# Optimization experiments

Hardware: AMD Instinct MI355X
Metric: run time of the kernel (lower is better)

The kernel has to match this reference:

```python
import jax, jax.numpy as jnp
import numpy as np

B, HH, WW = 4, 192, 192
DIM, HEADS, WIN, SHIFT, HID = 256, 8, 8, 4, 1024
EPS = 1e-5


def _rel_index(w):
    coords = np.stack(np.meshgrid(np.arange(w), np.arange(w), indexing='ij')).reshape(2, -1)
    rel = coords[:, :, None] - coords[:, None, :]            # [2, N, N]
    rel = rel.transpose(1, 2, 0).astype(np.int64)
    rel[:, :, 0] += w - 1
    rel[:, :, 1] += w - 1
    rel[:, :, 0] *= 2 * w - 1
    return rel.sum(-1)                                        # [N, N]


def _ln(x, g, b):
    m = x.mean(-1, keepdims=True)
    v = ((x - m) ** 2).mean(-1, keepdims=True)
    return (x - m) / jnp.sqrt(v + EPS) * g + b


def setup_inputs() -> dict:
    key = jax.random.key(0)
    ks = jax.random.split(key, 8)
    s = 0.02
    return {
        'x': jax.random.normal(ks[0], (B, HH * WW, DIM), jnp.float32),
        'norm1_g': jnp.ones((DIM,), jnp.float32),
        'norm1_b': jnp.zeros((DIM,), jnp.float32),
        'qkv_w': s * jax.random.normal(ks[1], (DIM, 3 * DIM), jnp.float32),
        'qkv_b': jnp.zeros((3 * DIM,), jnp.float32),
        'bias_table': s * jax.random.normal(ks[2], ((2 * WIN - 1) ** 2, HEADS), jnp.float32),
        'proj_w': s * jax.random.normal(ks[3], (DIM, DIM), jnp.float32),
        'proj_b': jnp.zeros((DIM,), jnp.float32),
        'norm2_g': jnp.ones((DIM,), jnp.float32),
        'norm2_b': jnp.zeros((DIM,), jnp.float32),
        'fc1_w': s * jax.random.normal(ks[4], (DIM, HID), jnp.float32),
        'fc1_b': jnp.zeros((HID,), jnp.float32),
        'fc2_w': s * jax.random.normal(ks[5], (HID, DIM), jnp.float32),
        'fc2_b': jnp.zeros((DIM,), jnp.float32),
        'H': HH,
        'W': WW,
    }


def reference(x, norm1_g, norm1_b, qkv_w, qkv_b, bias_table, proj_w, proj_b,
              norm2_g, norm2_b, fc1_w, fc1_b, fc2_w, fc2_b, H, W):
    Bn, L, C = x.shape
    hd = C // HEADS
    win = min(WIN, H, W)
    shift = SHIFT if win > SHIFT else 0
    shortcut = x

    h = _ln(x, norm1_g, norm1_b).reshape(Bn, H, W, C)
    pad_b = (win - H % win) % win
    pad_r = (win - W % win) % win
    h = jnp.pad(h, ((0, 0), (0, pad_b), (0, pad_r), (0, 0)))
    Hp, Wp = H + pad_b, W + pad_r
    if shift > 0:
        h = jnp.roll(h, (-shift, -shift), axis=(1, 2))

    nh, nw = Hp // win, Wp // win
    h = h.reshape(Bn, nh, win, nw, win, C).transpose(0, 1, 3, 2, 4, 5)
    h = h.reshape(Bn * nh * nw, win * win, C)
    N = win * win

    # windowed attention
    qkv = (h @ qkv_w + qkv_b).reshape(-1, N, 3, HEADS, hd)
    q, k, v = qkv[:, :, 0], qkv[:, :, 1], qkv[:, :, 2]      # [Bw, N, H, hd]
    scale = hd ** -0.5
    attn = jnp.einsum('bqhd,bkhd->bhqk', q * scale, k)
    rel_idx = jnp.asarray(_rel_index(win))                   # [N, N]
    bias = bias_table[rel_idx.reshape(-1)].reshape(N, N, HEADS).transpose(2, 0, 1)
    attn = jax.nn.softmax(attn + bias[None], axis=-1)
    o = jnp.einsum('bhqk,bkhd->bqhd', attn, v).reshape(-1, N, C)
    o = o @ proj_w + proj_b

    # window reverse
    o = o.reshape(Bn, nh, nw, win, win, C).transpose(0, 1, 3, 2, 4, 5).reshape(Bn, Hp, Wp, C)
    if shift > 0:
        o = jnp.roll(o, (shift, shift), axis=(1, 2))
    o = o[:, :H, :W, :].reshape(Bn, H * W, C)

    x = shortcut + o
    m = _ln(x, norm2_g, norm2_b)
    m = jax.nn.gelu(m @ fc1_w + fc1_b, approximate=False) @ fc2_w + fc2_b
    return x + m
```

## Files before the change

### kernel.cpp

```cpp
#include <hip/hip_runtime.h>


#define SHIFT_ 4

typedef __attribute__((ext_vector_type(8))) short short8;
typedef __attribute__((ext_vector_type(4))) float floatx4;

__device__ __forceinline__ unsigned short f2b(float f) {
  union { float f; unsigned int i; } c; c.f = f;
  unsigned int u = c.i;
  return (unsigned short)((u + 0x7FFFu + ((u >> 16) & 1u)) >> 16);
}

__device__ __forceinline__ float fast_gelu(float v) {
  const float u = v * v;
  const float z = v * (2.3022082f + 0.10294326f * u);
  const float e = __builtin_amdgcn_exp2f(z);
  const float r = __builtin_amdgcn_rcpf(1.f + e);
  return v - v * r;
}

__device__ __forceinline__ void load_lds16(const void* g, void* l) {
  __builtin_amdgcn_global_load_lds((__attribute__((address_space(1))) void*)g,
                                   (__attribute__((address_space(3))) void*)l, 16, 0, 0);
}

__device__ __forceinline__ size_t tok_of_row(int row) {
  int widx = row >> 6, t = row & 63;
  int b = widx / 576; int rem = widx - b * 576;
  int wy = rem / 24, wx = rem - wy * 24;
  int ti = t >> 3, tj = t & 7;
  int gr = wy * 8 + ti + SHIFT_; if (gr >= 192) gr -= 192;
  int gc = wx * 8 + tj + SHIFT_; if (gc >= 192) gc -= 192;
  return (size_t)b * 36864 + (size_t)(gr * 192 + gc);
}

template<int SHUFFLE>
__global__ __launch_bounds__(256) void ln_kernel(const float* __restrict__ src,
    const float* __restrict__ gw, const float* __restrict__ bw,
    unsigned short* __restrict__ dst) {
  const int lane = threadIdx.x & 63;
  const int m = blockIdx.x * 4 + (threadIdx.x >> 6);
  const size_t soff = SHUFFLE ? tok_of_row(m) * 256 : (size_t)m * 256;
  float4 xv = *(const float4*)(src + soff + lane * 4);
  float s  = xv.x + xv.y + xv.z + xv.w;
  float s2 = xv.x * xv.x + xv.y * xv.y + xv.z * xv.z + xv.w * xv.w;
  #pragma unroll
  for (int off = 32; off > 0; off >>= 1) { s += __shfl_xor(s, off); s2 += __shfl_xor(s2, off); }
  const float mean = s * 0.00390625f;
  const float var  = s2 * 0.00390625f - mean * mean;
  const float rstd = rsqrtf(var + 1e-5f);
  float4 gv = *(const float4*)(gw + lane * 4);
  float4 bv = *(const float4*)(bw + lane * 4);
  ushort4 o;
  o.x = f2b((xv.x - mean) * rstd * gv.x + bv.x);
  o.y = f2b((xv.y - mean) * rstd * gv.y + bv.y);
  o.z = f2b((xv.z - mean) * rstd * gv.z + bv.z);
  o.w = f2b((xv.w - mean) * rstd * gv.w + bv.w);
  *(ushort4*)(dst + (size_t)m * 256 + lane * 4) = o;
}

__global__ void wconv(const float* __restrict__ W, unsigned short* __restrict__ Wt,
                      int K, int N) {
  const int idx = blockIdx.x * 256 + threadIdx.x;
  const int n = idx / K, k = idx - n * K;
  Wt[idx] = f2b(W[(size_t)k * N + n]);
}

template<int MODE>
__global__ __launch_bounds__(256) void gemm_bt(
    const unsigned short* __restrict__ A, const unsigned short* __restrict__ Wt,
    const float* __restrict__ bias, const float* __restrict__ X,
    unsigned short* __restrict__ outb, float* __restrict__ outf,
    int Ntot, int K) {
  __shared__ unsigned short sm[16384];
  const int tid = threadIdx.x;
  const int wave = tid >> 6, lane = tid & 63;
  const int lr = lane & 15, lg = lane >> 4;
  const int wm = wave >> 1, wn = wave & 1;
  const int m0 = blockIdx.y * 128, n0 = blockIdx.x * 128;

  const unsigned short* rbase = (wave < 2) ? (A + (size_t)m0 * K)
                                           : (Wt + (size_t)n0 * K);
  unsigned short* ldsbase = &sm[wave * 4096];
  const int rc0 = (wave & 1) * 8;
  int off[8];
  #pragma unroll
  for (int t = 0; t < 8; ++t) {
    const int P = (rc0 + t) * 64 + lane;
    const int r = P >> 3, c = (P & 7) ^ (r & 7);
    off[t] = r * K + c * 8;
  }

  floatx4 acc[4][4];
  #pragma unroll
  for (int i = 0; i < 4; ++i)
    #pragma unroll
    for (int j = 0; j < 4; ++j) acc[i][j] = (floatx4)0.f;

  for (int k0 = 0; k0 < K; k0 += 64) {
    __syncthreads();
    #pragma unroll
    for (int t = 0; t < 8; ++t)
      load_lds16(rbase + (off[t] + k0), ldsbase + t * 512);
    __syncthreads();
    #pragma unroll
    for (int kk = 0; kk < 2; ++kk) {
      short8 af[4], bf[4];
      #pragma unroll
      for (int mi = 0; mi < 4; ++mi) {
        const int r = wm * 64 + mi * 16 + lr;
        af[mi] = *(const short8*)&sm[r * 64 + (((kk * 4 + lg) ^ (r & 7)) * 8)];
      }
      #pragma unroll
      for (int ni = 0; ni < 4; ++ni) {
        const int r = wn * 64 + ni * 16 + lr;
        bf[ni] = *(const short8*)&sm[8192 + r * 64 + (((kk * 4 + lg) ^ (r & 7)) * 8)];
      }
      #pragma unroll
      for (int mi = 0; mi < 4; ++mi)
        #pragma unroll
        for (int ni = 0; ni < 4; ++ni)
          acc[mi][ni] = __builtin_amdgcn_mfma_f32_16x16x32_bf16(af[mi], bf[ni], acc[mi][ni], 0, 0, 0);
    }
  }

  #pragma unroll
  for (int mi = 0; mi < 4; ++mi) {
    #pragma unroll
    for (int r = 0; r < 4; ++r) {
      const int row = m0 + wm * 64 + mi * 16 + lg * 4 + r;
      size_t obase;
      if (MODE == 1) obase = tok_of_row(row) * 256;
      else obase = (size_t)row * Ntot;
      #pragma unroll
      for (int ni = 0; ni < 4; ++ni) {
        const int col = n0 + wn * 64 + ni * 16 + lr;
        const float v = acc[mi][ni][r] + bias[col];
        if (MODE == 0) {
          outb[obase + col] = f2b(v);
        } else if (MODE == 1) {
          outf[obase + col] = X[obase + col] + v;
        } else if (MODE == 2) {
          outb[obase + col] = f2b(fast_gelu(v));
        } else {
          outf[obase + col] = X[obase + col] + v;
        }
      }
    }
  }
}

__global__ __launch_bounds__(64) void attn_kernel(const unsigned short* __restrict__ qkv,
    const float* __restrict__ btab, unsigned short* __restrict__ obuf) {
  __shared__ unsigned short vts[2048];
  __shared__ unsigned short ps[4096];
  __shared__ float bs[225];
  const int l = threadIdx.x;
  const int win = blockIdx.x >> 3, head = blockIdx.x & 7;
  const int lr = l & 15, lg = l >> 4;
  const unsigned short* base = qkv + (size_t)(win * 64) * 768 + head * 32;

  #pragma unroll
  for (int c = 0; c < 8; ++c) {
    ushort4 vv = *(const ushort4*)(base + (size_t)l * 768 + 512 + c * 4);
    #pragma unroll
    for (int j = 0; j < 4; ++j) {
      const int d = c * 4 + j;
      const unsigned short val = j == 0 ? vv.x : j == 1 ? vv.y : j == 2 ? vv.z : vv.w;
      vts[d * 64 + (((l >> 3) ^ (d & 7)) * 8) + (l & 7)] = val;
    }
  }
  for (int i = l; i < 225; i += 64) bs[i] = btab[i * 8 + head];

  short8 af[4], bfr[4];
  #pragma unroll
  for (int mi = 0; mi < 4; ++mi)
    af[mi] = *(const short8*)(base + (size_t)(mi * 16 + lr) * 768 + lg * 8);
  #pragma unroll
  for (int ni = 0; ni < 4; ++ni)
    bfr[ni] = *(const short8*)(base + (size_t)(ni * 16 + lr) * 768 + 256 + lg * 8);

  floatx4 sa[4][4];
  #pragma unroll
  for (int mi = 0; mi < 4; ++mi)
    #pragma unroll
    for (int ni = 0; ni < 4; ++ni)
      sa[mi][ni] = __builtin_amdgcn_mfma_f32_16x16x32_bf16(af[mi], bfr[ni], (floatx4)0.f, 0, 0, 0);

  __syncthreads();

  const float scale = 0.17677669529663687f;
  #pragma unroll
  for (int mi = 0; mi < 4; ++mi) {
    #pragma unroll
    for (int r = 0; r < 4; ++r) {
      const int qi = mi * 16 + lg * 4 + r;
      const int ti = qi >> 3, tj = qi & 7;
      float vals[4];
      #pragma unroll
      for (int ni = 0; ni < 4; ++ni) {
        const int kc = ni * 16 + lr;
        const int tk = kc >> 3, tl = kc & 7;
        vals[ni] = sa[mi][ni][r] * scale + bs[(ti - tk + 7) * 15 + (tj - tl + 7)];
      }
      float mx = fmaxf(fmaxf(vals[0], vals[1]), fmaxf(vals[2], vals[3]));
      #pragma unroll
      for (int off = 1; off < 16; off <<= 1) mx = fmaxf(mx, __shfl_xor(mx, off, 16));
      float se = 0.f;
      #pragma unroll
      for (int ni = 0; ni < 4; ++ni) { vals[ni] = __expf(vals[ni] - mx); se += vals[ni]; }
      #pragma unroll
      for (int off = 1; off < 16; off <<= 1) se += __shfl_xor(se, off, 16);
      const float inv = 1.f / se;
      #pragma unroll
      for (int ni = 0; ni < 4; ++ni) {
        const int col = ni * 16 + lr;
        const int cell = col >> 3;
        ps[qi * 64 + ((cell ^ (qi & 7)) * 8) + (col & 7)] = f2b(vals[ni] * inv);
      }
    }
  }
  __syncthreads();

  floatx4 oa[4][2];
  #pragma unroll
  for (int mi = 0; mi < 4; ++mi) { oa[mi][0] = (floatx4)0.f; oa[mi][1] = (floatx4)0.f; }
  #pragma unroll
  for (int kk = 0; kk < 2; ++kk) {
    short8 pa[4], vb[2];
    #pragma unroll
    for (int mi = 0; mi < 4; ++mi) {
      const int r = mi * 16 + lr;
      pa[mi] = *(const short8*)&ps[r * 64 + (((kk * 4 + lg) ^ (r & 7)) * 8)];
    }
    #pragma unroll
    for (int nj = 0; nj < 2; ++nj) {
      const int r = nj * 16 + lr;
      vb[nj] = *(const short8*)&vts[r * 64 + (((kk * 4 + lg) ^ (r & 7)) * 8)];
    }
    #pragma unroll
    for (int mi = 0; mi < 4; ++mi)
      #pragma unroll
      for (int nj = 0; nj < 2; ++nj)
        oa[mi][nj] = __builtin_amdgcn_mfma_f32_16x16x32_bf16(pa[mi], vb[nj], oa[mi][nj], 0, 0, 0);
  }
  #pragma unroll
  for (int mi = 0; mi < 4; ++mi)
    #pragma unroll
    for (int nj = 0; nj < 2; ++nj)
      #pragma unroll
      for (int r = 0; r < 4; ++r) {
        const int row = mi * 16 + lg * 4 + r, d = nj * 16 + lr;
        obuf[(size_t)(win * 64 + row) * 256 + head * 32 + d] = f2b(oa[mi][nj][r]);
      }
}

extern "C" void kernel_launch(void* const* d_in, const int* in_sizes, int n_in,
                              void* d_out, int out_size, void* d_ws, size_t ws_size,
                              hipStream_t stream) {
  (void)in_sizes; (void)n_in; (void)out_size; (void)ws_size;
  const float* x      = (const float*)d_in[0];
  const float* n1g    = (const float*)d_in[1];
  const float* n1b    = (const float*)d_in[2];
  const float* qkv_w  = (const float*)d_in[3];
  const float* qkv_b  = (const float*)d_in[4];
  const float* btab   = (const float*)d_in[5];
  const float* proj_w = (const float*)d_in[6];
  const float* proj_b = (const float*)d_in[7];
  const float* n2g    = (const float*)d_in[8];
  const float* n2b    = (const float*)d_in[9];
  const float* fc1_w  = (const float*)d_in[10];
  const float* fc1_b  = (const float*)d_in[11];
  const float* fc2_w  = (const float*)d_in[12];
  const float* fc2_b  = (const float*)d_in[13];
  float* out = (float*)d_out;

  char* wsb = (char*)d_ws;
  unsigned short* wqkv  = (unsigned short*)(wsb);
  unsigned short* wproj = (unsigned short*)(wsb + 393216);
  unsigned short* wfc1  = (unsigned short*)(wsb + 524288);
  unsigned short* wfc2  = (unsigned short*)(wsb + 1048576);
  unsigned short* hbuf  = (unsigned short*)(wsb + 1572864);
  unsigned short* big   = (unsigned short*)(wsb + 77070336);

  wconv<<<768, 256, 0, stream>>>(qkv_w, wqkv, 256, 768);
  wconv<<<256, 256, 0, stream>>>(proj_w, wproj, 256, 256);
  wconv<<<1024, 256, 0, stream>>>(fc1_w, wfc1, 256, 1024);
  wconv<<<1024, 256, 0, stream>>>(fc2_w, wfc2, 1024, 256);

  ln_kernel<1><<<36864, 256, 0, stream>>>(x, n1g, n1b, hbuf);
  gemm_bt<0><<<dim3(6, 1152), 256, 0, stream>>>(hbuf, wqkv, qkv_b, nullptr, big, nullptr, 768, 256);
  attn_kernel<<<18432, 64, 0, stream>>>(big, btab, hbuf);
  gemm_bt<1><<<dim3(2, 1152), 256, 0, stream>>>(hbuf, wproj, proj_b, x, nullptr, out, 256, 256);
  ln_kernel<0><<<36864, 256, 0, stream>>>(out, n2g, n2b, hbuf);
  gemm_bt<2><<<dim3(8, 1152), 256, 0, stream>>>(hbuf, wfc1, fc1_b, nullptr, big, nullptr, 1024, 256);
  gemm_bt<3><<<dim3(2, 1152), 256, 0, stream>>>(big, wfc2, fc2_b, out, nullptr, out, 256, 1024);
}
```

Before: 963.6 us.

## Fuse LayerNorm2, FC1+GELU and FC2 into a single MLP kernel

```diff
diff --git a/kernel.cpp b/kernel.cpp
--- a/kernel.cpp
+++ b/kernel.cpp
@@ -139,16 +139,136 @@
         const float v = acc[mi][ni][r] + bias[col];
         if (MODE == 0) {
           outb[obase + col] = f2b(v);
-        } else if (MODE == 1) {
-          outf[obase + col] = X[obase + col] + v;
-        } else if (MODE == 2) {
-          outb[obase + col] = f2b(fast_gelu(v));
         } else {
           outf[obase + col] = X[obase + col] + v;
         }
       }
     }
   }
+}
+
+__global__ __launch_bounds__(256, 2) void mlp_fused(
+    float* xio, const float* __restrict__ gw, const float* __restrict__ bw,
+    const unsigned short* __restrict__ w1, const float* __restrict__ b1,
+    const unsigned short* __restrict__ w2, const float* __restrict__ b2) {
+  __shared__ unsigned short smA[16384];
+  __shared__ unsigned short smH[16384];
+  const int tid = threadIdx.x;
+  const int wave = tid >> 6, lane = tid & 63;
+  const int lr = lane & 15, lg = lane >> 4;
+  const int m0 = blockIdx.x * 64;
+
+  {
+    const float4 gv = *(const float4*)(gw + lane * 4);
+    const float4 bv = *(const float4*)(bw + lane * 4);
+    for (int rr = 0; rr < 16; ++rr) {
+      const int row = wave * 16 + rr;
+      float4 xv = *(const float4*)(xio + (size_t)(m0 + row) * 256 + lane * 4);
+      float s  = xv.x + xv.y + xv.z + xv.w;
+      float s2 = xv.x * xv.x + xv.y * xv.y + xv.z * xv.z + xv.w * xv.w;
+      #pragma unroll
+      for (int off = 32; off > 0; off >>= 1) { s += __shfl_xor(s, off); s2 += __shfl_xor(s2, off); }
+      const float mean = s * 0.00390625f;
+      const float var  = s2 * 0.00390625f - mean * mean;
+      const float rstd = rsqrtf(var + 1e-5f);
+      ushort4 o;
+      o.x = f2b((xv.x - mean) * rstd * gv.x + bv.x);
+      o.y = f2b((xv.y - mean) * rstd * gv.y + bv.y);
+      o.z = f2b((xv.z - mean) * rstd * gv.z + bv.z);
+      o.w = f2b((xv.w - mean) * rstd * gv.w + bv.w);
+      const int idx = row * 256 + ((((lane >> 1) ^ (row & 7))) << 3) + (lane & 1) * 4;
+      *(ushort4*)&smA[idx] = o;
+    }
+  }
+  __syncthreads();
+
+  float b2v[4];
+  #pragma unroll
+  for (int ni = 0; ni < 4; ++ni) b2v[ni] = b2[wave * 64 + ni * 16 + lr];
+
+  floatx4 acc2[4][4];
+  #pragma unroll
+  for (int i = 0; i < 4; ++i)
+    #pragma unroll
+    for (int j = 0; j < 4; ++j) acc2[i][j] = (floatx4)0.f;
+
+  for (int q = 0; q < 4; ++q) {
+    floatx4 acc1[4][4];
+    #pragma unroll
+    for (int i = 0; i < 4; ++i)
+      #pragma unroll
+      for (int j = 0; j < 4; ++j) acc1[i][j] = (floatx4)0.f;
+
+    const unsigned short* w1q = w1 + (size_t)(q * 256 + wave * 64) * 256;
+    #pragma unroll
+    for (int kk = 0; kk < 8; ++kk) {
+      short8 af[4], bf[4];
+      #pragma unroll
+      for (int mi = 0; mi < 4; ++mi) {
+        const int r = mi * 16 + lr;
+        af[mi] = *(const short8*)&smA[r * 256 + (((kk * 4 + lg) ^ (r & 7)) << 3)];
+      }
+      #pragma unroll
+      for (int ni = 0; ni < 4; ++ni)
+        bf[ni] = *(const short8*)(w1q + (ni * 16 + lr) * 256 + kk * 32 + lg * 8);
+      #pragma unroll
+      for (int mi = 0; mi < 4; ++mi)
+        #pragma unroll
+        for (int ni = 0; ni < 4; ++ni)
+          acc1[mi][ni] = __builtin_amdgcn_mfma_f32_16x16x32_bf16(af[mi], bf[ni], acc1[mi][ni], 0, 0, 0);
+    }
+
+    float b1v[4];
+    #pragma unroll
+    for (int ni = 0; ni < 4; ++ni) b1v[ni] = b1[q * 256 + wave * 64 + ni * 16 + lr];
+
+    __syncthreads();
+    #pragma unroll
+    for (int mi = 0; mi < 4; ++mi)
+      #pragma unroll
+      for (int r = 0; r < 4; ++r) {
+        const int row = mi * 16 + lg * 4 + r;
+        const int rbase = row * 256, rx = row & 7;
+        #pragma unroll
+        for (int ni = 0; ni < 4; ++ni) {
+          const int col = wave * 64 + ni * 16 + lr;
+          const float v = acc1[mi][ni][r] + b1v[ni];
+          smH[rbase + (((col >> 3) ^ rx) << 3) + (lr & 7)] = f2b(fast_gelu(v));
+        }
+      }
+    __syncthreads();
+
+    const unsigned short* w2q = w2 + q * 256;
+    #pragma unroll
+    for (int kk = 0; kk < 8; ++kk) {
+      short8 af[4], bf[4];
+      #pragma unroll
+      for (int mi = 0; mi < 4; ++mi) {
+        const int r = mi * 16 + lr;
+        af[mi] = *(const short8*)&smH[r * 256 + (((kk * 4 + lg) ^ (r & 7)) << 3)];
+      }
+      #pragma unroll
+      for (int ni = 0; ni < 4; ++ni)
+        bf[ni] = *(const short8*)(w2q + (size_t)(wave * 64 + ni * 16 + lr) * 1024 + kk * 32 + lg * 8);
+      #pragma unroll
+      for (int mi = 0; mi < 4; ++mi)
+        #pragma unroll
+        for (int ni = 0; ni < 4; ++ni)
+          acc2[mi][ni] = __builtin_amdgcn_mfma_f32_16x16x32_bf16(af[mi], bf[ni], acc2[mi][ni], 0, 0, 0);
+    }
+  }
+
+  #pragma unroll
+  for (int mi = 0; mi < 4; ++mi)
+    #pragma unroll
+    for (int r = 0; r < 4; ++r) {
+      const size_t gbase = (size_t)(m0 + mi * 16 + lg * 4 + r) * 256;
+      #pragma unroll
+      for (int ni = 0; ni < 4; ++ni) {
+        const int col = wave * 64 + ni * 16 + lr;
+        xio[gbase + col] += acc2[mi][ni][r] + b2v[ni];
+      }
+    }
 }
 
 __global__ __launch_bounds__(64) void attn_kernel(const unsigned short* __restrict__ qkv,
@@ -293,7 +413,5 @@
   gemm_bt<0><<<dim3(6, 1152), 256, 0, stream>>>(hbuf, wqkv, qkv_b, nullptr, big, nullptr, 768, 256);
   attn_kernel<<<18432, 64, 0, stream>>>(big, btab, hbuf);
   gemm_bt<1><<<dim3(2, 1152), 256, 0, stream>>>(hbuf, wproj, proj_b, x, nullptr, out, 256, 256);
-  ln_kernel<0><<<36864, 256, 0, stream>>>(out, n2g, n2b, hbuf);
-  gemm_bt<2><<<dim3(8, 1152), 256, 0, stream>>>(hbuf, wfc1, fc1_b, nullptr, big, nullptr, 1024, 256);
-  gemm_bt<3><<<dim3(2, 1152), 256, 0, stream>>>(big, wfc2, fc2_b, out, nullptr, out, 256, 1024);
-}
+  mlp_fused<<<2304, 256, 0, stream>>>(out, n2g, n2b, wfc1, fc1_b, wfc2, fc2_b);
+}
```

After: 978.5 us. About the same (+1.5%).
